# Kernel tuning notes

Measured on AMD Instinct MI355X. Metric: run time of the kernel, lower is better.

Reference implementation:

```python
import jax, jax.numpy as jnp
import numpy as np

# Model dims (eval mode: dropout off, no gate noise, no KV cache, start_pos=0)
B, T, C = 2, 2048, 1024
H, KV = 16, 4
HD = C // H            # 64
E, K = 8, 2            # n_experts, active_experts
FE, FS = 1024, 2048    # expert_inter_dim, shared inter_dim
EPS = 1e-6
BASE = 10000.0


def setup_inputs() -> dict:
    key = jax.random.key(0)
    ks = jax.random.split(key, 15)
    s = 0.02
    f32 = jnp.float32
    return {
        'x': jax.random.normal(ks[0], (B, T, C), f32),
        'norm1_w': jnp.ones((C,), f32),
        'norm2_w': jnp.ones((C,), f32),
        'wq': jax.random.normal(ks[1], (C, H * HD), f32) * s,
        'wk': jax.random.normal(ks[2], (C, KV * HD), f32) * s,
        'wv': jax.random.normal(ks[3], (C, KV * HD), f32) * s,
        'wo': jax.random.normal(ks[4], (H * HD, C), f32) * s,
        'gate_w': jax.random.normal(ks[5], (C, E), f32) * s,
        'exp_w1': jax.random.normal(ks[6], (E, C, FE), f32) * s,
        'exp_w2': jax.random.normal(ks[7], (E, C, FE), f32) * s,
        'exp_wp': jax.random.normal(ks[8], (E, FE, C), f32) * s,
        'sh_w1': jax.random.normal(ks[9], (C, FS), f32) * s,
        'sh_w2': jax.random.normal(ks[10], (C, FS), f32) * s,
        'sh_wp': jax.random.normal(ks[11], (FS, C), f32) * s,
    }


def _rms(x, w):
    return x * jax.lax.rsqrt(jnp.mean(x * x, -1, keepdims=True) + EPS) * w


def _rope_table(t, hd):
    freqs = 1.0 / (BASE ** (jnp.arange(0, hd, 2, dtype=jnp.float32) / hd))
    ang = jnp.outer(jnp.arange(t, dtype=jnp.float32), freqs)  # (T, hd/2)
    return jnp.stack([jnp.cos(ang), jnp.sin(ang)], -1)        # (T, hd/2, 2)


def _apply_rope(x, fc):
    # x: (B, T, nH, hd); fc: (T, hd/2, 2)
    xr = x.reshape(*x.shape[:-1], -1, 2)
    cos = fc[None, :, None, :, 0]
    sin = fc[None, :, None, :, 1]
    out = jnp.stack([xr[..., 0] * cos - xr[..., 1] * sin,
                     xr[..., 1] * cos + xr[..., 0] * sin], -1)
    return out.reshape(x.shape).astype(x.dtype)


def reference(x, norm1_w, norm2_w, wq, wk, wv, wo, gate_w,
              exp_w1, exp_w2, exp_wp, sh_w1, sh_w2, sh_wp):
    fc = _rope_table(T, HD)
    # --- GQA attention with RoPE ---
    h1 = _rms(x, norm1_w)
    q = (h1 @ wq).reshape(B, T, H, HD)
    k = (h1 @ wk).reshape(B, T, KV, HD)
    v = (h1 @ wv).reshape(B, T, KV, HD)
    q = _apply_rope(q, fc)
    k = _apply_rope(k, fc)
    rep = H // KV
    k = jnp.repeat(k, rep, axis=2)  # (B,T,H,HD)
    v = jnp.repeat(v, rep, axis=2)
    scores = jnp.einsum('bqhd,bkhd->bhqk', q, k) / jnp.sqrt(jnp.float32(HD))
    mask = jnp.where(jnp.tril(jnp.ones((T, T), bool)), 0.0, -1e9).astype(scores.dtype)
    att = jax.nn.softmax(scores + mask, axis=-1)
    o = jnp.einsum('bhqk,bkhd->bqhd', att, v).reshape(B, T, C) @ wo
    x1 = x + o
    # --- MoE block (top-k gate, dense masked combine == gather/scatter math) ---
    h2 = _rms(x1, norm2_w).reshape(-1, C)  # (N, C), N = B*T
    gate_logits = h2 @ gate_w              # (N, E)
    p = jax.nn.softmax(gate_logits, axis=-1)
    topw, topi = jax.lax.top_k(p, K)       # values == gather(p, indices)
    comb = jnp.sum(jax.nn.one_hot(topi, E, dtype=p.dtype) * topw[..., None], axis=1)  # (N, E)
    he = jax.nn.silu(jnp.einsum('nc,ecf->enf', h2, exp_w1)) * jnp.einsum('nc,ecf->enf', h2, exp_w2)
    ye = jnp.einsum('enf,efc->enc', he, exp_wp)
    y = jnp.einsum('enc,ne->nc', ye, comb)
    z = (jax.nn.silu(h2 @ sh_w1) * (h2 @ sh_w2)) @ sh_wp
    out = x1 + (y + z).reshape(B, T, C)
    return out, gate_logits
```

## Files before the change

kernel.cpp:

```cpp
#include <hip/hip_runtime.h>
#include <hip/hip_bf16.h>

#define TB 2
#define TT 2048
#define TC 1024
#define TH 16
#define TKV 4
#define THD 64
#define TE 8
#define TFE 1024
#define TFS 2048
#define NTOK 4096
#define NSLOT 8192

typedef __attribute__((ext_vector_type(4))) float f32x4;
typedef __attribute__((ext_vector_type(16))) float f32x16;
typedef __attribute__((ext_vector_type(8))) short s16x8;

__device__ __forceinline__ float bf2f(short s) {
    unsigned int u = ((unsigned int)(unsigned short)s) << 16;
    return __builtin_bit_cast(float, u);
}
__device__ __forceinline__ short f2bf(float f) {
    unsigned int u = __builtin_bit_cast(unsigned int, f);
    u = u + 0x7fffu + ((u >> 16) & 1u);
    return (short)(u >> 16);
}
__device__ __forceinline__ unsigned int cvtpk_bf16(float lo, float hi) {
    unsigned int r;
    asm volatile("v_cvt_pk_bf16_f32 %0, %1, %2" : "=v"(r) : "v"(lo), "v"(hi));
    return r;
}

__device__ __forceinline__ void gl_lds16(const void* g, void* l) {
    __builtin_amdgcn_global_load_lds((const __attribute__((address_space(1))) void*)g,
                                     (__attribute__((address_space(3))) void*)l,
                                     16, 0, 0);
}

__global__ __launch_bounds__(256) void k_transp(const float* __restrict__ in,
                                                short* __restrict__ out,
                                                int R, int Cd,
                                                size_t bs_in, size_t bs_out) {
    __shared__ float tile[32][33];
    const float* ip = in + bs_in * blockIdx.z;
    short* op = out + bs_out * blockIdx.z;
    int tx = threadIdx.x & 31, ty = threadIdx.x >> 5;
    int r0 = blockIdx.y * 32, c0 = blockIdx.x * 32;
    #pragma unroll
    for (int r = ty; r < 32; r += 8)
        tile[r][tx] = ip[(size_t)(r0 + r) * Cd + c0 + tx];
    __syncthreads();
    #pragma unroll
    for (int r = ty; r < 32; r += 8)
        op[(size_t)(c0 + r) * R + r0 + tx] = f2bf(tile[tx][r]);
}

__global__ __launch_bounds__(256) void k_transp_v(const short* __restrict__ qkv,
                                                  short* __restrict__ v_t) {
    __shared__ short tile[32][33];
    int z = blockIdx.z;
    int b = z >> 2, kvh = z & 3;
    const short* ip = qkv + (size_t)b * TT * 1536 + 1280 + kvh * 64;
    short* op = v_t + (size_t)z * THD * TT;
    int tx = threadIdx.x & 31, ty = threadIdx.x >> 5;
    int t0 = blockIdx.y * 32, d0 = blockIdx.x * 32;
    #pragma unroll
    for (int r = ty; r < 32; r += 8)
        tile[r][tx] = ip[(size_t)(t0 + r) * 1536 + d0 + tx];
    __syncthreads();
    #pragma unroll
    for (int r = ty; r < 32; r += 8)
        op[(size_t)(d0 + r) * TT + t0 + tx] = tile[tx][r];
}

__global__ void k_rope_table(float* __restrict__ rope) {
    int idx = blockIdx.x * 256 + threadIdx.x;
    if (idx >= TT * 32) return;
    int t = idx >> 5, i = idx & 31;
    float freq = expf(-(float)i * (1.0f / 32.0f) * 9.210340371976184f);
    float ang = (float)t * freq;
    rope[idx * 2 + 0] = cosf(ang);
    rope[idx * 2 + 1] = sinf(ang);
}

__global__ __launch_bounds__(256) void k_rmsnorm(const float* __restrict__ x,
                                                 const float* __restrict__ w,
                                                 short* __restrict__ out) {
    int row = blockIdx.x, t = threadIdx.x;
    float4 v = ((const float4*)(x + (size_t)row * TC))[t];
    float ss = v.x * v.x + v.y * v.y + v.z * v.z + v.w * v.w;
    #pragma unroll
    for (int off = 32; off; off >>= 1) ss += __shfl_xor(ss, off);
    __shared__ float red[4];
    if ((t & 63) == 0) red[t >> 6] = ss;
    __syncthreads();
    float rs = rsqrtf((red[0] + red[1] + red[2] + red[3]) * (1.0f / 1024.0f) + 1e-6f);
    float4 wv = ((const float4*)w)[t];
    short4 o;
    o.x = f2bf(v.x * rs * wv.x);
    o.y = f2bf(v.y * rs * wv.y);
    o.z = f2bf(v.z * rs * wv.z);
    o.w = f2bf(v.w * rs * wv.w);
    ((short4*)(out + (size_t)row * TC))[t] = o;
}

template <int EPI>
__global__ __launch_bounds__(256) void k_gemm128(const short* __restrict__ A,
                                                 const short* __restrict__ Bt,
                                                 void* __restrict__ outp,
                                                 const float* __restrict__ resid,
                                                 int M, int N, int K) {
    __shared__ short As[128 * 32];
    __shared__ short Bs[128 * 32];
    int tid = threadIdx.x;
    int brow = blockIdx.y * 128, bcol = blockIdx.x * 128;
    int wid = tid >> 6, lane = tid & 63;
    int wr = wid >> 1, wc = wid & 1, g = lane >> 4, c = lane & 15;
    int srow = wid * 32 + (lane >> 2);
    int scol = (lane & 3) * 8;
    const short* Ag0 = A + (size_t)(brow + srow) * K + scol;
    const short* Ag1 = A + (size_t)(brow + srow + 16) * K + scol;
    const short* Bg0 = Bt + (size_t)(bcol + srow) * K + scol;
    const short* Bg1 = Bt + (size_t)(bcol + srow + 16) * K + scol;
    int loff = __builtin_amdgcn_readfirstlane(wid * 2048);
    char* Al0 = (char*)As + loff;
    char* Bl0 = (char*)Bs + loff;
    f32x4 acc[4][4] = {};
    for (int kk = 0; kk < K; kk += 32) {
        __syncthreads();
        gl_lds16(Ag0 + kk, Al0);
        gl_lds16(Ag1 + kk, Al0 + 1024);
        gl_lds16(Bg0 + kk, Bl0);
        gl_lds16(Bg1 + kk, Bl0 + 1024);
        __syncthreads();
        s16x8 af[4], bf[4];
        #pragma unroll
        for (int m = 0; m < 4; m++) af[m] = *(const s16x8*)(As + (wr * 64 + m * 16 + c) * 32 + g * 8);
        #pragma unroll
        for (int n = 0; n < 4; n++) bf[n] = *(const s16x8*)(Bs + (wc * 64 + n * 16 + c) * 32 + g * 8);
        #pragma unroll
        for (int m = 0; m < 4; m++)
            #pragma unroll
            for (int n = 0; n < 4; n++)
                acc[m][n] = __builtin_amdgcn_mfma_f32_16x16x32_bf16(af[m], bf[n], acc[m][n], 0, 0, 0);
    }
    #pragma unroll
    for (int m = 0; m < 4; m++)
        #pragma unroll
        for (int n = 0; n < 4; n++)
            #pragma unroll
            for (int j = 0; j < 4; j++) {
                int row = brow + wr * 64 + m * 16 + g * 4 + j;
                int col = bcol + wc * 64 + n * 16 + c;
                float v = acc[m][n][j];
                if (EPI == 0)
                    ((short*)outp)[(size_t)row * N + col] = f2bf(v);
                else
                    ((float*)outp)[(size_t)row * N + col] = v + resid[(size_t)row * N + col];
            }
}

template <int EPI>
__global__ __launch_bounds__(256) void k_gemm64(const short* __restrict__ A,
                                                const short* __restrict__ Bt,
                                                void* __restrict__ outp,
                                                const float* __restrict__ resid,
                                                int M, int N, int K) {
    __shared__ short As[128 * 32];
    __shared__ short Bs[64 * 32];
    int tid = threadIdx.x;
    int brow = blockIdx.y * 128, bcol = blockIdx.x * 64;
    int wid = tid >> 6, lane = tid & 63;
    int wr = wid >> 1, wc = wid & 1, g = lane >> 4, c = lane & 15;
    int srow = wid * 32 + (lane >> 2);
    int scol = (lane & 3) * 8;
    const short* Ag0 = A + (size_t)(brow + srow) * K + scol;
    const short* Ag1 = A + (size_t)(brow + srow + 16) * K + scol;
    int sbrow = wid * 16 + (lane >> 2);
    const short* Bg = Bt + (size_t)(bcol + sbrow) * K + scol;
    int loffA = __builtin_amdgcn_readfirstlane(wid * 2048);
    int loffB = __builtin_amdgcn_readfirstlane(wid * 1024);
    char* Al = (char*)As + loffA;
    char* Bl = (char*)Bs + loffB;
    f32x4 acc[4][2] = {};
    for (int kk = 0; kk < K; kk += 32) {
        __syncthreads();
        gl_lds16(Ag0 + kk, Al);
        gl_lds16(Ag1 + kk, Al + 1024);
        gl_lds16(Bg + kk, Bl);
        __syncthreads();
        s16x8 af[4], bf[2];
        #pragma unroll
        for (int m = 0; m < 4; m++) af[m] = *(const s16x8*)(As + (wr * 64 + m * 16 + c) * 32 + g * 8);
        #pragma unroll
        for (int n = 0; n < 2; n++) bf[n] = *(const s16x8*)(Bs + (wc * 32 + n * 16 + c) * 32 + g * 8);
        #pragma unroll
        for (int m = 0; m < 4; m++)
            #pragma unroll
            for (int n = 0; n < 2; n++)
                acc[m][n] = __builtin_amdgcn_mfma_f32_16x16x32_bf16(af[m], bf[n], acc[m][n], 0, 0, 0);
    }
    #pragma unroll
    for (int m = 0; m < 4; m++)
        #pragma unroll
        for (int n = 0; n < 2; n++)
            #pragma unroll
            for (int j = 0; j < 4; j++) {
                int row = brow + wr * 64 + m * 16 + g * 4 + j;
                int col = bcol + wc * 32 + n * 16 + c;
                float v = acc[m][n][j];
                if (EPI == 0)
                    ((short*)outp)[(size_t)row * N + col] = f2bf(v);
                else
                    ((float*)outp)[(size_t)row * N + col] = v + resid[(size_t)row * N + col];
            }
}

__global__ void k_rope_apply(const short* __restrict__ qkv,
                             const float* __restrict__ rope,
                             short* __restrict__ q_r,
                             short* __restrict__ k_r) {
    int idx = blockIdx.x * 256 + threadIdx.x;
    if (idx >= NTOK * 640) return;
    int row = idx / 640;
    int p = idx - row * 640;
    int b = row >> 11, t = row & 2047;
    const short* src = qkv + (size_t)row * 1536;
    if (p < 512) {
        int h = p >> 5, i = p & 31;
        float x0 = bf2f(src[h * 64 + 2 * i]);
        float x1 = bf2f(src[h * 64 + 2 * i + 1]);
        float cs = rope[(t * 32 + i) * 2], sn = rope[(t * 32 + i) * 2 + 1];
        size_t o = ((size_t)(b * TH + h) * TT + t) * THD + 2 * i;
        q_r[o]     = f2bf(x0 * cs - x1 * sn);
        q_r[o + 1] = f2bf(x1 * cs + x0 * sn);
    } else {
        int pk = p - 512;
        int kv = pk >> 5, i = pk & 31;
        float x0 = bf2f(src[1024 + kv * 64 + 2 * i]);
        float x1 = bf2f(src[1024 + kv * 64 + 2 * i + 1]);
        float cs = rope[(t * 32 + i) * 2], sn = rope[(t * 32 + i) * 2 + 1];
        size_t o = ((size_t)(b * TKV + kv) * TT + t) * THD + 2 * i;
        k_r[o]     = f2bf(x0 * cs - x1 * sn);
        k_r[o + 1] = f2bf(x1 * cs + x0 * sn);
    }
}

__global__ __launch_bounds__(256) void k_attn(const short* __restrict__ q_r,
                                              const short* __restrict__ k_r,
                                              const short* __restrict__ v_t,
                                              short* __restrict__ attn_o) {
    int w = threadIdx.x >> 6, lane = threadIdx.x & 63;
    int qt = 63 - (blockIdx.x * 4 + w);
    int qbase = qt * 32;
    int bh = blockIdx.y;
    int b = bh >> 4, h = bh & 15, kv = h >> 2;
    int q32 = lane & 31, hi = lane >> 5;

    const short* qp = q_r + ((size_t)(b * TH + h) * TT + qbase) * THD;
    const short* kp = k_r + ((size_t)(b * TKV + kv) * TT) * THD;
    const short* vp = v_t + ((size_t)(b * TKV + kv) * THD) * TT;

    s16x8 qf[4];
    #pragma unroll
    for (int dc = 0; dc < 4; dc++)
        qf[dc] = *(const s16x8*)(qp + q32 * THD + dc * 16 + hi * 8);

    f32x16 ot0 = {}, ot1 = {};
    float mrun = -1e30f, lrun = 0.f;
    int nkt = (qbase + 95) >> 6;

    for (int kt = 0; kt < nkt; kt++) {
        int ktb = kt * 64;
        f32x16 st0 = {}, st1 = {};
        s16x8 kf0[4], kf1[4];
        #pragma unroll
        for (int dc = 0; dc < 4; dc++) {
            kf0[dc] = *(const s16x8*)(kp + (size_t)(ktb + q32) * THD + dc * 16 + hi * 8);
            kf1[dc] = *(const s16x8*)(kp + (size_t)(ktb + 32 + q32) * THD + dc * 16 + hi * 8);
        }
        s16x8 vf[8];
        #pragma unroll
        for (int dt = 0; dt < 2; dt++)
            #pragma unroll
            for (int kc = 0; kc < 4; kc++)
                vf[dt * 4 + kc] = *(const s16x8*)(vp + (size_t)(dt * 32 + q32) * TT + ktb + kc * 16 + hi * 8);

        __builtin_amdgcn_s_setprio(1);
        #pragma unroll
        for (int dc = 0; dc < 4; dc++) {
            st0 = __builtin_amdgcn_mfma_f32_32x32x16_bf16(kf0[dc], qf[dc], st0, 0, 0, 0);
            st1 = __builtin_amdgcn_mfma_f32_32x32x16_bf16(kf1[dc], qf[dc], st1, 0, 0, 0);
        }
        __builtin_amdgcn_s_setprio(0);

        bool domask = (kt == nkt - 1);
        int qabs = qbase + q32;
        #pragma unroll
        for (int r = 0; r < 16; r++) {
            int kploc = (r & 3) + 8 * (r >> 2) + 4 * hi;
            float s0 = st0[r] * 0.125f;
            float s1 = st1[r] * 0.125f;
            if (domask) {
                if (ktb + kploc > qabs) s0 = -1e30f;
                if (ktb + 32 + kploc > qabs) s1 = -1e30f;
            }
            st0[r] = s0; st1[r] = s1;
        }
        float pm = st0[0];
        #pragma unroll
        for (int r = 1; r < 16; r++) pm = fmaxf(pm, st0[r]);
        #pragma unroll
        for (int r = 0; r < 16; r++) pm = fmaxf(pm, st1[r]);
        pm = fmaxf(pm, __shfl_xor(pm, 32));
        float mnew = fmaxf(mrun, pm);
        float al = __expf(mrun - mnew);
        mrun = mnew;
        float rs = 0.f;
        #pragma unroll
        for (int r = 0; r < 16; r++) {
            float e0 = __expf(st0[r] - mnew); st0[r] = e0; rs += e0;
            float e1 = __expf(st1[r] - mnew); st1[r] = e1; rs += e1;
        }
        rs += __shfl_xor(rs, 32);
        lrun = lrun * al + rs;
        #pragma unroll
        for (int r = 0; r < 16; r++) { ot0[r] *= al; ot1[r] *= al; }

        unsigned int w0[8], w1[8];
        #pragma unroll
        for (int j = 0; j < 8; j++) {
            w0[j] = cvtpk_bf16(st0[2 * j], st0[2 * j + 1]);
            w1[j] = cvtpk_bf16(st1[2 * j], st1[2 * j + 1]);
        }
        s16x8 pf[4];
        #pragma unroll
        for (int kc = 0; kc < 4; kc++) {
            unsigned int* ww = (kc < 2) ? w0 : w1;
            int kcl = kc & 1;
            unsigned int x0 = ww[4 * kcl + 0], y0 = ww[4 * kcl + 2];
            unsigned int x1 = ww[4 * kcl + 1], y1 = ww[4 * kcl + 3];
            asm volatile("v_permlane32_swap_b32 %0, %1" : "+v"(x0), "+v"(y0));
            asm volatile("v_permlane32_swap_b32 %0, %1" : "+v"(x1), "+v"(y1));
            unsigned int fr[4] = {x0, x1, y0, y1};
            pf[kc] = __builtin_bit_cast(s16x8, *(ulong2*)fr);
        }
        __builtin_amdgcn_s_setprio(1);
        #pragma unroll
        for (int kc = 0; kc < 4; kc++) {
            ot0 = __builtin_amdgcn_mfma_f32_32x32x16_bf16(vf[kc], pf[kc], ot0, 0, 0, 0);
            ot1 = __builtin_amdgcn_mfma_f32_32x32x16_bf16(vf[4 + kc], pf[kc], ot1, 0, 0, 0);
        }
        __builtin_amdgcn_s_setprio(0);
    }
    float inv = 1.0f / lrun;
    short* orow = attn_o + (size_t)(b * TT + qbase + q32) * TC + h * THD;
    #pragma unroll
    for (int s = 0; s < 4; s++) {
        short4 v0, v1;
        v0.x = f2bf(ot0[4 * s + 0] * inv); v0.y = f2bf(ot0[4 * s + 1] * inv);
        v0.z = f2bf(ot0[4 * s + 2] * inv); v0.w = f2bf(ot0[4 * s + 3] * inv);
        v1.x = f2bf(ot1[4 * s + 0] * inv); v1.y = f2bf(ot1[4 * s + 1] * inv);
        v1.z = f2bf(ot1[4 * s + 2] * inv); v1.w = f2bf(ot1[4 * s + 3] * inv);
        *(short4*)(orow + 8 * s + 4 * hi) = v0;
        *(short4*)(orow + 32 + 8 * s + 4 * hi) = v1;
    }
}

__global__ __launch_bounds__(256) void k_gate(const float* __restrict__ x1,
                                              const float* __restrict__ n2w,
                                              const float* __restrict__ gate_w,
                                              float* __restrict__ gl,
                                              int* __restrict__ cnt,
                                              int* __restrict__ te,
                                              int* __restrict__ tls,
                                              float* __restrict__ tw) {
    int w = threadIdx.x >> 6, lane = threadIdx.x & 63;
    int n = blockIdx.x * 4 + w;
    const float* xp = x1 + (size_t)n * TC;
    float ss = 0.f;
    for (int i = lane; i < TC; i += 64) { float v = xp[i]; ss += v * v; }
    #pragma unroll
    for (int off = 32; off; off >>= 1) ss += __shfl_xor(ss, off);
    float rs = rsqrtf(ss * (1.0f / 1024.0f) + 1e-6f);
    int e = lane & 7, ch = lane >> 3;
    float acc = 0.f;
    for (int i = 0; i < 128; i++) {
        int cc = ch * 128 + i;
        acc += xp[cc] * rs * n2w[cc] * gate_w[(size_t)cc * TE + e];
    }
    acc += __shfl_xor(acc, 8);
    acc += __shfl_xor(acc, 16);
    acc += __shfl_xor(acc, 32);
    float logit = acc;
    if (lane < 8) gl[(size_t)n * TE + lane] = logit;
    float mx = logit;
    mx = fmaxf(mx, __shfl_xor(mx, 1)); mx = fmaxf(mx, __shfl_xor(mx, 2)); mx = fmaxf(mx, __shfl_xor(mx, 4));
    float ex = __expf(logit - mx);
    float sm = ex;
    sm += __shfl_xor(sm, 1); sm += __shfl_xor(sm, 2); sm += __shfl_xor(sm, 4);
    float pp = ex / sm;
    float m1 = pp;
    m1 = fmaxf(m1, __shfl_xor(m1, 1)); m1 = fmaxf(m1, __shfl_xor(m1, 2)); m1 = fmaxf(m1, __shfl_xor(m1, 4));
    int cand = (pp == m1) ? e : 8;
    int e0 = cand;
    e0 = min(e0, __shfl_xor(e0, 1)); e0 = min(e0, __shfl_xor(e0, 2)); e0 = min(e0, __shfl_xor(e0, 4));
    float p2 = (e == e0) ? -1.0f : pp;
    float m2 = p2;
    m2 = fmaxf(m2, __shfl_xor(m2, 1)); m2 = fmaxf(m2, __shfl_xor(m2, 2)); m2 = fmaxf(m2, __shfl_xor(m2, 4));
    int cand2 = (p2 == m2) ? e : 8;
    int e1 = cand2;
    e1 = min(e1, __shfl_xor(e1, 1)); e1 = min(e1, __shfl_xor(e1, 2)); e1 = min(e1, __shfl_xor(e1, 4));
    if (lane == 0) {
        int ls0 = atomicAdd(&cnt[e0], 1);
        int ls1 = atomicAdd(&cnt[e1], 1);
        te[n * 2] = e0; te[n * 2 + 1] = e1;
        tls[n * 2] = ls0; tls[n * 2 + 1] = ls1;
        tw[n * 2] = m1; tw[n * 2 + 1] = m2;
    }
}

__global__ void k_prefix(const int* __restrict__ cnt, int* __restrict__ basep) {
    if (threadIdx.x == 0) {
        int s = 0;
        for (int e = 0; e < TE; e++) { basep[e] = s; s += cnt[e]; }
    }
}

__global__ void k_scatter(const int* __restrict__ te, const int* __restrict__ tls,
                          const float* __restrict__ tw, const int* __restrict__ basep,
                          int* __restrict__ tlist, float* __restrict__ slotw,
                          int* __restrict__ sot) {
    int n = blockIdx.x * 256 + threadIdx.x;
    if (n >= NTOK) return;
    int s0 = basep[te[n * 2]] + tls[n * 2];
    int s1 = basep[te[n * 2 + 1]] + tls[n * 2 + 1];
    tlist[s0] = n; tlist[s1] = n;
    slotw[s0] = tw[n * 2]; slotw[s1] = tw[n * 2 + 1];
    sot[n * 2] = s0; sot[n * 2 + 1] = s1;
}

__global__ __launch_bounds__(512) void k_ffn(const short* __restrict__ A,
                                             const short* __restrict__ eB1,
                                             const short* __restrict__ eB2,
                                             const short* __restrict__ sB1,
                                             const short* __restrict__ sB2,
                                             short* __restrict__ he,
                                             short* __restrict__ shm,
                                             const int* __restrict__ cnt,
                                             const int* __restrict__ basep,
                                             const int* __restrict__ tlist,
                                             const float* __restrict__ slotw) {
    int z = blockIdx.z;
    int moe = (z < 8);
    int nt = blockIdx.x, mt = blockIdx.y;
    int ce = 0, base = 0;
    if (moe) {
        if (nt >= 8) return;
        ce = cnt[z];
        if (mt * 128 >= ce) return;
        base = basep[z];
    }
    __shared__ short As[128 * 32];
    __shared__ short B1s[128 * 32];
    __shared__ short B2s[128 * 32];
    int tid = threadIdx.x, wid = tid >> 6, lane = tid & 63;
    int wr = wid >> 2, wc = wid & 3, g = lane >> 4, c = lane & 15;
    const int K = TC;
    int srow = wid * 16 + (lane >> 2);
    int scol = (lane & 3) * 8;
    size_t arow;
    if (moe) {
        int l0 = mt * 128 + srow; if (l0 >= ce) l0 = ce - 1;
        arow = (size_t)tlist[base + l0];
    } else {
        arow = (size_t)(mt * 128 + srow);
    }
    const short* Ag = A + arow * (size_t)K + scol;
    const short* B1g;
    const short* B2g;
    if (moe) {
        B1g = eB1 + ((size_t)z * TFE + (size_t)(nt * 128 + srow)) * K + scol;
        B2g = eB2 + ((size_t)z * TFE + (size_t)(nt * 128 + srow)) * K + scol;
    } else {
        B1g = sB1 + (size_t)(nt * 128 + srow) * K + scol;
        B2g = sB2 + (size_t)(nt * 128 + srow) * K + scol;
    }
    int loff = __builtin_amdgcn_readfirstlane(wid * 1024);
    char* Al = (char*)As + loff;
    char* B1l = (char*)B1s + loff;
    char* B2l = (char*)B2s + loff;
    f32x4 a1[4][2] = {}, a2[4][2] = {};
    for (int kk = 0; kk < K; kk += 32) {
        __syncthreads();
        gl_lds16(Ag + kk, Al);
        gl_lds16(B1g + kk, B1l);
        gl_lds16(B2g + kk, B2l);
        __syncthreads();
        s16x8 af[4], b1[2], b2[2];
        #pragma unroll
        for (int m_ = 0; m_ < 4; m_++) af[m_] = *(const s16x8*)(As + (wr * 64 + m_ * 16 + c) * 32 + g * 8);
        #pragma unroll
        for (int n = 0; n < 2; n++) {
            b1[n] = *(const s16x8*)(B1s + (wc * 32 + n * 16 + c) * 32 + g * 8);
            b2[n] = *(const s16x8*)(B2s + (wc * 32 + n * 16 + c) * 32 + g * 8);
        }
        #pragma unroll
        for (int m_ = 0; m_ < 4; m_++)
            #pragma unroll
            for (int n = 0; n < 2; n++) {
                a1[m_][n] = __builtin_amdgcn_mfma_f32_16x16x32_bf16(af[m_], b1[n], a1[m_][n], 0, 0, 0);
                a2[m_][n] = __builtin_amdgcn_mfma_f32_16x16x32_bf16(af[m_], b2[n], a2[m_][n], 0, 0, 0);
            }
    }
    #pragma unroll
    for (int m_ = 0; m_ < 4; m_++)
        #pragma unroll
        for (int n = 0; n < 2; n++)
            #pragma unroll
            for (int j = 0; j < 4; j++) {
                int lrow = mt * 128 + wr * 64 + m_ * 16 + g * 4 + j;
                if (moe && lrow >= ce) continue;
                int col = nt * 128 + wc * 32 + n * 16 + c;
                float g1 = a1[m_][n][j], g2 = a2[m_][n][j];
                float v = g1 / (1.0f + __expf(-g1)) * g2;
                if (moe) {
                    v *= slotw[base + lrow];
                    he[(size_t)(base + lrow) * TFE + col] = f2bf(v);
                } else {
                    shm[(size_t)lrow * TFS + col] = f2bf(v);
                }
            }
}

__global__ __launch_bounds__(256) void k_moe2(const short* __restrict__ he,
                                              const short* __restrict__ Wpt,
                                              short* __restrict__ ye,
                                              const int* __restrict__ cnt,
                                              const int* __restrict__ basep) {
    int e = blockIdx.z;
    int ce = cnt[e];
    int mt = blockIdx.y;
    if (mt * 128 >= ce) return;
    int base = basep[e];
    int nt = blockIdx.x;
    __shared__ short As[128 * 32];
    __shared__ short Bs[128 * 32];
    int tid = threadIdx.x, wid = tid >> 6, lane = tid & 63;
    int wr = wid >> 1, wc = wid & 1, g = lane >> 4, c = lane & 15;
    int srow = wid * 32 + (lane >> 2);
    int scol = (lane & 3) * 8;
    const short* Ag0 = he + (size_t)(base + mt * 128 + srow) * TFE + scol;
    const short* Ag1 = Ag0 + (size_t)16 * TFE;
    const short* Bg0 = Wpt + ((size_t)e * 1024 + nt * 128 + srow) * TFE + scol;
    const short* Bg1 = Bg0 + (size_t)16 * TFE;
    int loff = __builtin_amdgcn_readfirstlane(wid * 2048);
    char* Al = (char*)As + loff;
    char* Bl = (char*)Bs + loff;
    f32x4 acc[4][4] = {};
    for (int kk = 0; kk < TFE; kk += 32) {
        __syncthreads();
        gl_lds16(Ag0 + kk, Al);
        gl_lds16(Ag1 + kk, Al + 1024);
        gl_lds16(Bg0 + kk, Bl);
        gl_lds16(Bg1 + kk, Bl + 1024);
        __syncthreads();
        s16x8 af[4], bf[4];
        #pragma unroll
        for (int m = 0; m < 4; m++) af[m] = *(const s16x8*)(As + (wr * 64 + m * 16 + c) * 32 + g * 8);
        #pragma unroll
        for (int n = 0; n < 4; n++) bf[n] = *(const s16x8*)(Bs + (wc * 64 + n * 16 + c) * 32 + g * 8);
        #pragma unroll
        for (int m = 0; m < 4; m++)
            #pragma unroll
            for (int n = 0; n < 4; n++)
                acc[m][n] = __builtin_amdgcn_mfma_f32_16x16x32_bf16(af[m], bf[n], acc[m][n], 0, 0, 0);
    }
    #pragma unroll
    for (int m = 0; m < 4; m++)
        #pragma unroll
        for (int n = 0; n < 4; n++)
            #pragma unroll
            for (int j = 0; j < 4; j++) {
                int lrow = mt * 128 + wr * 64 + m * 16 + g * 4 + j;
                if (lrow >= ce) continue;
                int col = nt * 128 + wc * 64 + n * 16 + c;
                ye[(size_t)(base + lrow) * TC + col] = f2bf(acc[m][n][j]);
            }
}

__global__ __launch_bounds__(256) void k_final(const short* __restrict__ A,
                                               const short* __restrict__ Bt,
                                               const float* __restrict__ x1,
                                               const short* __restrict__ ye,
                                               const int* __restrict__ sot,
                                               float* __restrict__ outp) {
    __shared__ short As[128 * 32];
    __shared__ short Bs[64 * 32];
    const int K = TFS;
    int tid = threadIdx.x;
    int brow = blockIdx.y * 128, bcol = blockIdx.x * 64;
    int wid = tid >> 6, lane = tid & 63;
    int wr = wid >> 1, wc = wid & 1, g = lane >> 4, c = lane & 15;
    int srow = wid * 32 + (lane >> 2);
    int scol = (lane & 3) * 8;
    const short* Ag0 = A + (size_t)(brow + srow) * K + scol;
    const short* Ag1 = A + (size_t)(brow + srow + 16) * K + scol;
    int sbrow = wid * 16 + (lane >> 2);
    const short* Bg = Bt + (size_t)(bcol + sbrow) * K + scol;
    int loffA = __builtin_amdgcn_readfirstlane(wid * 2048);
    int loffB = __builtin_amdgcn_readfirstlane(wid * 1024);
    char* Al = (char*)As + loffA;
    char* Bl = (char*)Bs + loffB;
    f32x4 acc[4][2] = {};
    for (int kk = 0; kk < K; kk += 32) {
        __syncthreads();
        gl_lds16(Ag0 + kk, Al);
        gl_lds16(Ag1 + kk, Al + 1024);
        gl_lds16(Bg + kk, Bl);
        __syncthreads();
        s16x8 af[4], bf[2];
        #pragma unroll
        for (int m = 0; m < 4; m++) af[m] = *(const s16x8*)(As + (wr * 64 + m * 16 + c) * 32 + g * 8);
        #pragma unroll
        for (int n = 0; n < 2; n++) bf[n] = *(const s16x8*)(Bs + (wc * 32 + n * 16 + c) * 32 + g * 8);
        #pragma unroll
        for (int m = 0; m < 4; m++)
            #pragma unroll
            for (int n = 0; n < 2; n++)
                acc[m][n] = __builtin_amdgcn_mfma_f32_16x16x32_bf16(af[m], bf[n], acc[m][n], 0, 0, 0);
    }
    #pragma unroll
    for (int m = 0; m < 4; m++)
        #pragma unroll
        for (int n = 0; n < 2; n++)
            #pragma unroll
            for (int j = 0; j < 4; j++) {
                int row = brow + wr * 64 + m * 16 + g * 4 + j;
                int col = bcol + wc * 32 + n * 16 + c;
                int s0 = sot[row * 2], s1 = sot[row * 2 + 1];
                float v = acc[m][n][j] + x1[(size_t)row * TC + col]
                        + bf2f(ye[(size_t)s0 * TC + col]) + bf2f(ye[(size_t)s1 * TC + col]);
                outp[(size_t)row * TC + col] = v;
            }
}

extern "C" void kernel_launch(void* const* d_in, const int* in_sizes, int n_in,
                              void* d_out, int out_size, void* d_ws, size_t ws_size,
                              hipStream_t stream) {
    const float* x     = (const float*)d_in[0];
    const float* n1w   = (const float*)d_in[1];
    const float* n2w   = (const float*)d_in[2];
    const float* wq    = (const float*)d_in[3];
    const float* wk    = (const float*)d_in[4];
    const float* wv    = (const float*)d_in[5];
    const float* wo    = (const float*)d_in[6];
    const float* gatew = (const float*)d_in[7];
    const float* ew1   = (const float*)d_in[8];
    const float* ew2   = (const float*)d_in[9];
    const float* ewp   = (const float*)d_in[10];
    const float* sw1   = (const float*)d_in[11];
    const float* sw2   = (const float*)d_in[12];
    const float* swp   = (const float*)d_in[13];
    float* outp = (float*)d_out;

    char* p = (char*)d_ws;
    auto alloc = [&](size_t bytes) -> char* {
        char* r = p;
        p += (bytes + 255) & ~(size_t)255;
        return r;
    };
    short* wqkv_t = (short*)alloc(1536 * 1024 * 2);
    short* wo_t   = (short*)alloc(1024 * 1024 * 2);
    short* ew1_t  = (short*)alloc((size_t)8 * 1024 * 1024 * 2);
    short* ew2_t  = (short*)alloc((size_t)8 * 1024 * 1024 * 2);
    short* ewp_t  = (short*)alloc((size_t)8 * 1024 * 1024 * 2);
    short* sw1_t  = (short*)alloc((size_t)2048 * 1024 * 2);
    short* sw2_t  = (short*)alloc((size_t)2048 * 1024 * 2);
    short* swp_t  = (short*)alloc((size_t)1024 * 2048 * 2);
    short* h1     = (short*)alloc((size_t)NTOK * 1024 * 2);
    short* qkv    = (short*)alloc((size_t)NTOK * 1536 * 2);
    short* q_r    = (short*)alloc((size_t)TB * TH * TT * THD * 2);
    short* k_r    = (short*)alloc((size_t)TB * TKV * TT * THD * 2);
    short* v_t    = (short*)alloc((size_t)TB * TKV * THD * TT * 2);
    short* attn_o = (short*)alloc((size_t)NTOK * 1024 * 2);
    float* x1     = (float*)alloc((size_t)NTOK * 1024 * 4);
    short* h2     = (short*)alloc((size_t)NTOK * 1024 * 2);
    float* rope   = (float*)alloc((size_t)TT * 32 * 2 * 4);
    int*   cnt    = (int*)alloc(256);
    int*   basep  = (int*)alloc(256);
    int*   te     = (int*)alloc((size_t)NTOK * 2 * 4);
    int*   tls    = (int*)alloc((size_t)NTOK * 2 * 4);
    float* tw     = (float*)alloc((size_t)NTOK * 2 * 4);
    int*   tlist  = (int*)alloc((size_t)NSLOT * 4);
    float* slotw  = (float*)alloc((size_t)NSLOT * 4);
    int*   sot    = (int*)alloc((size_t)NTOK * 2 * 4);
    short* he     = (short*)alloc((size_t)NSLOT * TFE * 2);
    short* ye     = (short*)alloc((size_t)NSLOT * TC * 2);
    short* shm    = (short*)alloc((size_t)NTOK * TFS * 2);

    dim3 blk(256);

    k_transp<<<dim3(32, 32, 1), blk, 0, stream>>>(wq, wqkv_t, 1024, 1024, 0, 0);
    k_transp<<<dim3(8, 32, 1), blk, 0, stream>>>(wk, wqkv_t + 1024 * 1024, 1024, 256, 0, 0);
    k_transp<<<dim3(8, 32, 1), blk, 0, stream>>>(wv, wqkv_t + 1280 * 1024, 1024, 256, 0, 0);
    k_transp<<<dim3(32, 32, 1), blk, 0, stream>>>(wo, wo_t, 1024, 1024, 0, 0);
    k_transp<<<dim3(32, 32, 8), blk, 0, stream>>>(ew1, ew1_t, 1024, 1024, 1048576, 1048576);
    k_transp<<<dim3(32, 32, 8), blk, 0, stream>>>(ew2, ew2_t, 1024, 1024, 1048576, 1048576);
    k_transp<<<dim3(32, 32, 8), blk, 0, stream>>>(ewp, ewp_t, 1024, 1024, 1048576, 1048576);
    k_transp<<<dim3(64, 32, 1), blk, 0, stream>>>(sw1, sw1_t, 1024, 2048, 0, 0);
    k_transp<<<dim3(64, 32, 1), blk, 0, stream>>>(sw2, sw2_t, 1024, 2048, 0, 0);
    k_transp<<<dim3(32, 64, 1), blk, 0, stream>>>(swp, swp_t, 2048, 1024, 0, 0);

    k_rope_table<<<(TT * 32 + 255) / 256, blk, 0, stream>>>(rope);

    k_rmsnorm<<<NTOK, blk, 0, stream>>>(x, n1w, h1);
    k_gemm128<0><<<dim3(12, 32), blk, 0, stream>>>(h1, wqkv_t, qkv, nullptr, NTOK, 1536, 1024);
    k_rope_apply<<<(NTOK * 640 + 255) / 256, blk, 0, stream>>>(qkv, rope, q_r, k_r);
    k_transp_v<<<dim3(2, 64, 8), blk, 0, stream>>>(qkv, v_t);

    k_attn<<<dim3(16, TB * TH), blk, 0, stream>>>(q_r, k_r, v_t, attn_o);

    k_gemm64<1><<<dim3(16, 32), blk, 0, stream>>>(attn_o, wo_t, x1, x, NTOK, 1024, 1024);

    k_rmsnorm<<<NTOK, blk, 0, stream>>>(x1, n2w, h2);

    hipMemsetAsync(cnt, 0, 64, stream);
    k_gate<<<NTOK / 4, blk, 0, stream>>>(x1, n2w, gatew, outp + (size_t)NTOK * TC, cnt, te, tls, tw);
    k_prefix<<<1, 64, 0, stream>>>(cnt, basep);
    k_scatter<<<NTOK / 256, blk, 0, stream>>>(te, tls, tw, basep, tlist, slotw, sot);

    k_ffn<<<dim3(16, 32, 9), dim3(512), 0, stream>>>(h2, ew1_t, ew2_t, sw1_t, sw2_t, he, shm,
                                                     cnt, basep, tlist, slotw);
    k_moe2<<<dim3(8, 32, 8), blk, 0, stream>>>(he, ewp_t, ye, cnt, basep);

    k_final<<<dim3(16, 32), blk, 0, stream>>>(shm, swp_t, x1, ye, sot, outp);

    (void)in_sizes; (void)n_in; (void)out_size; (void)ws_size;
}
```

Before: 746.8 us.

## Double-buffer LDS tiles in all GEMM kernels to overlap loads with MFMA

Every bf16 GEMM kernel (the 128- and 64-wide GEMMs, the fused expert/shared up-projection, the expert down-projection and the final GEMM) now uses two LDS buffers per operand. The first tile is loaded before the loop. Each iteration starts the global-to-LDS load of the next K-tile while running MFMAs on the current one, and needs only one barrier per iteration instead of two. The aim is to hide global-load latency behind compute. In exchange, LDS use per block doubles, which may lower occupancy. The overlap also depends on the compiler not placing a full vmcnt wait before the LDS reads.

```diff
diff --git a/kernel.cpp b/kernel.cpp
--- a/kernel.cpp
+++ b/kernel.cpp
@@ -111,8 +111,8 @@
                                                  void* __restrict__ outp,
                                                  const float* __restrict__ resid,
                                                  int M, int N, int K) {
-    __shared__ short As[128 * 32];
-    __shared__ short Bs[128 * 32];
+    __shared__ short As0[128 * 32], As1[128 * 32];
+    __shared__ short Bs0[128 * 32], Bs1[128 * 32];
     int tid = threadIdx.x;
     int brow = blockIdx.y * 128, bcol = blockIdx.x * 128;
     int wid = tid >> 6, lane = tid & 63;
@@ -124,26 +124,38 @@
     const short* Bg0 = Bt + (size_t)(bcol + srow) * K + scol;
     const short* Bg1 = Bt + (size_t)(bcol + srow + 16) * K + scol;
     int loff = __builtin_amdgcn_readfirstlane(wid * 2048);
-    char* Al0 = (char*)As + loff;
-    char* Bl0 = (char*)Bs + loff;
     f32x4 acc[4][4] = {};
+
+    gl_lds16(Ag0, (char*)As0 + loff);
+    gl_lds16(Ag1, (char*)As0 + loff + 1024);
+    gl_lds16(Bg0, (char*)Bs0 + loff);
+    gl_lds16(Bg1, (char*)Bs0 + loff + 1024);
+    __syncthreads();
+
+    short* Ac = As0; short* Bc = Bs0;
+    short* Aa = As1; short* Ba = Bs1;
     for (int kk = 0; kk < K; kk += 32) {
-        __syncthreads();
-        gl_lds16(Ag0 + kk, Al0);
-        gl_lds16(Ag1 + kk, Al0 + 1024);
-        gl_lds16(Bg0 + kk, Bl0);
-        gl_lds16(Bg1 + kk, Bl0 + 1024);
-        __syncthreads();
+        int kn = kk + 32;
+        if (kn < K) {
+            gl_lds16(Ag0 + kn, (char*)Aa + loff);
+            gl_lds16(Ag1 + kn, (char*)Aa + loff + 1024);
+            gl_lds16(Bg0 + kn, (char*)Ba + loff);
+            gl_lds16(Bg1 + kn, (char*)Ba + loff + 1024);
+        }
         s16x8 af[4], bf[4];
         #pragma unroll
-        for (int m = 0; m < 4; m++) af[m] = *(const s16x8*)(As + (wr * 64 + m * 16 + c) * 32 + g * 8);
-        #pragma unroll
-        for (int n = 0; n < 4; n++) bf[n] = *(const s16x8*)(Bs + (wc * 64 + n * 16 + c) * 32 + g * 8);
+        for (int m = 0; m < 4; m++) af[m] = *(const s16x8*)(Ac + (wr * 64 + m * 16 + c) * 32 + g * 8);
+        #pragma unroll
+        for (int n = 0; n < 4; n++) bf[n] = *(const s16x8*)(Bc + (wc * 64 + n * 16 + c) * 32 + g * 8);
         #pragma unroll
         for (int m = 0; m < 4; m++)
             #pragma unroll
             for (int n = 0; n < 4; n++)
                 acc[m][n] = __builtin_amdgcn_mfma_f32_16x16x32_bf16(af[m], bf[n], acc[m][n], 0, 0, 0);
+        __syncthreads();
+        short* t;
+        t = Ac; Ac = Aa; Aa = t;
+        t = Bc; Bc = Ba; Ba = t;
     }
     #pragma unroll
     for (int m = 0; m < 4; m++)
@@ -167,8 +179,8 @@
                                                 void* __restrict__ outp,
                                                 const float* __restrict__ resid,
                                                 int M, int N, int K) {
-    __shared__ short As[128 * 32];
-    __shared__ short Bs[64 * 32];
+    __shared__ short As0[128 * 32], As1[128 * 32];
+    __shared__ short Bs0[64 * 32], Bs1[64 * 32];
     int tid = threadIdx.x;
     int brow = blockIdx.y * 128, bcol = blockIdx.x * 64;
     int wid = tid >> 6, lane = tid & 63;
@@ -181,25 +193,36 @@
     const short* Bg = Bt + (size_t)(bcol + sbrow) * K + scol;
     int loffA = __builtin_amdgcn_readfirstlane(wid * 2048);
     int loffB = __builtin_amdgcn_readfirstlane(wid * 1024);
-    char* Al = (char*)As + loffA;
-    char* Bl = (char*)Bs + loffB;
     f32x4 acc[4][2] = {};
+
+    gl_lds16(Ag0, (char*)As0 + loffA);
+    gl_lds16(Ag1, (char*)As0 + loffA + 1024);
+    gl_lds16(Bg, (char*)Bs0 + loffB);
+    __syncthreads();
+
+    short* Ac = As0; short* Bc = Bs0;
+    short* Aa = As1; short* Ba = Bs1;
     for (int kk = 0; kk < K; kk += 32) {
-        __syncthreads();
-        gl_lds16(Ag0 + kk, Al);
-        gl_lds16(Ag1 + kk, Al + 1024);
-        gl_lds16(Bg + kk, Bl);
-        __syncthreads();
+        int kn = kk + 32;
+        if (kn < K) {
+            gl_lds16(Ag0 + kn, (char*)Aa + loffA);
+            gl_lds16(Ag1 + kn, (char*)Aa + loffA + 1024);
+            gl_lds16(Bg + kn, (char*)Ba + loffB);
+        }
         s16x8 af[4], bf[2];
         #pragma unroll
-        for (int m = 0; m < 4; m++) af[m] = *(const s16x8*)(As + (wr * 64 + m * 16 + c) * 32 + g * 8);
-        #pragma unroll
-        for (int n = 0; n < 2; n++) bf[n] = *(const s16x8*)(Bs + (wc * 32 + n * 16 + c) * 32 + g * 8);
+        for (int m = 0; m < 4; m++) af[m] = *(const s16x8*)(Ac + (wr * 64 + m * 16 + c) * 32 + g * 8);
+        #pragma unroll
+        for (int n = 0; n < 2; n++) bf[n] = *(const s16x8*)(Bc + (wc * 32 + n * 16 + c) * 32 + g * 8);
         #pragma unroll
         for (int m = 0; m < 4; m++)
             #pragma unroll
             for (int n = 0; n < 2; n++)
                 acc[m][n] = __builtin_amdgcn_mfma_f32_16x16x32_bf16(af[m], bf[n], acc[m][n], 0, 0, 0);
+        __syncthreads();
+        short* t;
+        t = Ac; Ac = Aa; Aa = t;
+        t = Bc; Bc = Ba; Ba = t;
     }
     #pragma unroll
     for (int m = 0; m < 4; m++)
@@ -462,9 +485,9 @@
         if (mt * 128 >= ce) return;
         base = basep[z];
     }
-    __shared__ short As[128 * 32];
-    __shared__ short B1s[128 * 32];
-    __shared__ short B2s[128 * 32];
+    __shared__ short As0[128 * 32], As1[128 * 32];
+    __shared__ short B1s0[128 * 32], B1s1[128 * 32];
+    __shared__ short B2s0[128 * 32], B2s1[128 * 32];
     int tid = threadIdx.x, wid = tid >> 6, lane = tid & 63;
     int wr = wid >> 2, wc = wid & 3, g = lane >> 4, c = lane & 15;
     const int K = TC;
@@ -488,23 +511,29 @@
         B2g = sB2 + (size_t)(nt * 128 + srow) * K + scol;
     }
     int loff = __builtin_amdgcn_readfirstlane(wid * 1024);
-    char* Al = (char*)As + loff;
-    char* B1l = (char*)B1s + loff;
-    char* B2l = (char*)B2s + loff;
     f32x4 a1[4][2] = {}, a2[4][2] = {};
+
+    gl_lds16(Ag, (char*)As0 + loff);
+    gl_lds16(B1g, (char*)B1s0 + loff);
+    gl_lds16(B2g, (char*)B2s0 + loff);
+    __syncthreads();
+
+    short* Ac = As0;  short* B1c = B1s0;  short* B2c = B2s0;
+    short* Aa = As1;  short* B1a = B1s1;  short* B2a = B2s1;
     for (int kk = 0; kk < K; kk += 32) {
-        __syncthreads();
-        gl_lds16(Ag + kk, Al);
-        gl_lds16(B1g + kk, B1l);
-        gl_lds16(B2g + kk, B2l);
-        __syncthreads();
+        int kn = kk + 32;
+        if (kn < K) {
+            gl_lds16(Ag + kn, (char*)Aa + loff);
+            gl_lds16(B1g + kn, (char*)B1a + loff);
+            gl_lds16(B2g + kn, (char*)B2a + loff);
+        }
         s16x8 af[4], b1[2], b2[2];
         #pragma unroll
-        for (int m_ = 0; m_ < 4; m_++) af[m_] = *(const s16x8*)(As + (wr * 64 + m_ * 16 + c) * 32 + g * 8);
+        for (int m_ = 0; m_ < 4; m_++) af[m_] = *(const s16x8*)(Ac + (wr * 64 + m_ * 16 + c) * 32 + g * 8);
         #pragma unroll
         for (int n = 0; n < 2; n++) {
-            b1[n] = *(const s16x8*)(B1s + (wc * 32 + n * 16 + c) * 32 + g * 8);
-            b2[n] = *(const s16x8*)(B2s + (wc * 32 + n * 16 + c) * 32 + g * 8);
+            b1[n] = *(const s16x8*)(B1c + (wc * 32 + n * 16 + c) * 32 + g * 8);
+            b2[n] = *(const s16x8*)(B2c + (wc * 32 + n * 16 + c) * 32 + g * 8);
         }
         #pragma unroll
         for (int m_ = 0; m_ < 4; m_++)
@@ -513,6 +542,11 @@
                 a1[m_][n] = __builtin_amdgcn_mfma_f32_16x16x32_bf16(af[m_], b1[n], a1[m_][n], 0, 0, 0);
                 a2[m_][n] = __builtin_amdgcn_mfma_f32_16x16x32_bf16(af[m_], b2[n], a2[m_][n], 0, 0, 0);
             }
+        __syncthreads();
+        short* t;
+        t = Ac; Ac = Aa; Aa = t;
+        t = B1c; B1c = B1a; B1a = t;
+        t = B2c; B2c = B2a; B2a = t;
     }
     #pragma unroll
     for (int m_ = 0; m_ < 4; m_++)
@@ -545,8 +579,8 @@
     if (mt * 128 >= ce) return;
     int base = basep[e];
     int nt = blockIdx.x;
-    __shared__ short As[128 * 32];
-    __shared__ short Bs[128 * 32];
+    __shared__ short As0[128 * 32], As1[128 * 32];
+    __shared__ short Bs0[128 * 32], Bs1[128 * 32];
     int tid = threadIdx.x, wid = tid >> 6, lane = tid & 63;
     int wr = wid >> 1, wc = wid & 1, g = lane >> 4, c = lane & 15;
     int srow = wid * 32 + (lane >> 2);
@@ -556,26 +590,38 @@
     const short* Bg0 = Wpt + ((size_t)e * 1024 + nt * 128 + srow) * TFE + scol;
     const short* Bg1 = Bg0 + (size_t)16 * TFE;
     int loff = __builtin_amdgcn_readfirstlane(wid * 2048);
-    char* Al = (char*)As + loff;
-    char* Bl = (char*)Bs + loff;
     f32x4 acc[4][4] = {};
+
+    gl_lds16(Ag0, (char*)As0 + loff);
+    gl_lds16(Ag1, (char*)As0 + loff + 1024);
+    gl_lds16(Bg0, (char*)Bs0 + loff);
+    gl_lds16(Bg1, (char*)Bs0 + loff + 1024);
+    __syncthreads();
+
+    short* Ac = As0; short* Bc = Bs0;
+    short* Aa = As1; short* Ba = Bs1;
     for (int kk = 0; kk < TFE; kk += 32) {
-        __syncthreads();
-        gl_lds16(Ag0 + kk, Al);
-        gl_lds16(Ag1 + kk, Al + 1024);
-        gl_lds16(Bg0 + kk, Bl);
-        gl_lds16(Bg1 + kk, Bl + 1024);
-        __syncthreads();
+        int kn = kk + 32;
+        if (kn < TFE) {
+            gl_lds16(Ag0 + kn, (char*)Aa + loff);
+            gl_lds16(Ag1 + kn, (char*)Aa + loff + 1024);
+            gl_lds16(Bg0 + kn, (char*)Ba + loff);
+            gl_lds16(Bg1 + kn, (char*)Ba + loff + 1024);
+        }
         s16x8 af[4], bf[4];
         #pragma unroll
-        for (int m = 0; m < 4; m++) af[m] = *(const s16x8*)(As + (wr * 64 + m * 16 + c) * 32 + g * 8);
-        #pragma unroll
-        for (int n = 0; n < 4; n++) bf[n] = *(const s16x8*)(Bs + (wc * 64 + n * 16 + c) * 32 + g * 8);
+        for (int m = 0; m < 4; m++) af[m] = *(const s16x8*)(Ac + (wr * 64 + m * 16 + c) * 32 + g * 8);
+        #pragma unroll
+        for (int n = 0; n < 4; n++) bf[n] = *(const s16x8*)(Bc + (wc * 64 + n * 16 + c) * 32 + g * 8);
         #pragma unroll
         for (int m = 0; m < 4; m++)
             #pragma unroll
             for (int n = 0; n < 4; n++)
                 acc[m][n] = __builtin_amdgcn_mfma_f32_16x16x32_bf16(af[m], bf[n], acc[m][n], 0, 0, 0);
+        __syncthreads();
+        short* t;
+        t = Ac; Ac = Aa; Aa = t;
+        t = Bc; Bc = Ba; Ba = t;
     }
     #pragma unroll
     for (int m = 0; m < 4; m++)
@@ -596,8 +642,8 @@
                                                const short* __restrict__ ye,
                                                const int* __restrict__ sot,
                                                float* __restrict__ outp) {
-    __shared__ short As[128 * 32];
-    __shared__ short Bs[64 * 32];
+    __shared__ short As0[128 * 32], As1[128 * 32];
+    __shared__ short Bs0[64 * 32], Bs1[64 * 32];
     const int K = TFS;
     int tid = threadIdx.x;
     int brow = blockIdx.y * 128, bcol = blockIdx.x * 64;
@@ -611,25 +657,36 @@
     const short* Bg = Bt + (size_t)(bcol + sbrow) * K + scol;
     int loffA = __builtin_amdgcn_readfirstlane(wid * 2048);
     int loffB = __builtin_amdgcn_readfirstlane(wid * 1024);
-    char* Al = (char*)As + loffA;
-    char* Bl = (char*)Bs + loffB;
     f32x4 acc[4][2] = {};
+
+    gl_lds16(Ag0, (char*)As0 + loffA);
+    gl_lds16(Ag1, (char*)As0 + loffA + 1024);
+    gl_lds16(Bg, (char*)Bs0 + loffB);
+    __syncthreads();
+
+    short* Ac = As0; short* Bc = Bs0;
+    short* Aa = As1; short* Ba = Bs1;
     for (int kk = 0; kk < K; kk += 32) {
-        __syncthreads();
-        gl_lds16(Ag0 + kk, Al);
-        gl_lds16(Ag1 + kk, Al + 1024);
-        gl_lds16(Bg + kk, Bl);
-        __syncthreads();
+        int kn = kk + 32;
+        if (kn < K) {
+            gl_lds16(Ag0 + kn, (char*)Aa + loffA);
+            gl_lds16(Ag1 + kn, (char*)Aa + loffA + 1024);
+            gl_lds16(Bg + kn, (char*)Ba + loffB);
+        }
         s16x8 af[4], bf[2];
         #pragma unroll
-        for (int m = 0; m < 4; m++) af[m] = *(const s16x8*)(As + (wr * 64 + m * 16 + c) * 32 + g * 8);
-        #pragma unroll
-        for (int n = 0; n < 2; n++) bf[n] = *(const s16x8*)(Bs + (wc * 32 + n * 16 + c) * 32 + g * 8);
+        for (int m = 0; m < 4; m++) af[m] = *(const s16x8*)(Ac + (wr * 64 + m * 16 + c) * 32 + g * 8);
+        #pragma unroll
+        for (int n = 0; n < 2; n++) bf[n] = *(const s16x8*)(Bc + (wc * 32 + n * 16 + c) * 32 + g * 8);
         #pragma unroll
         for (int m = 0; m < 4; m++)
             #pragma unroll
             for (int n = 0; n < 2; n++)
                 acc[m][n] = __builtin_amdgcn_mfma_f32_16x16x32_bf16(af[m], bf[n], acc[m][n], 0, 0, 0);
+        __syncthreads();
+        short* t;
+        t = Ac; Ac = Aa; Aa = t;
+        t = Bc; Bc = Ba; Ba = t;
     }
     #pragma unroll
     for (int m = 0; m < 4; m++)
```

Measured after the change: 724.4 us. -3.0%, faster.
